# Performance work log

Hardware: AMD Instinct MI355X
Metric: run time of the kernel (lower is better)

Reference implementation:

```python
import jax, jax.numpy as jnp
import numpy as np

N_NODES = 100000
N_EDGES = 1600000
D_FEAT = 48


def setup_inputs() -> dict:
    key = jax.random.key(0)
    k1, k2, k3, k4 = jax.random.split(key, 4)
    rows = jax.random.randint(k1, (N_EDGES,), 0, N_NODES, dtype=jnp.int32)
    cols = jax.random.randint(k2, (N_EDGES,), 0, N_NODES, dtype=jnp.int32)
    vals = jax.random.uniform(k3, (N_EDGES,), dtype=jnp.float32)
    embeds = jax.random.normal(k4, (N_NODES, D_FEAT), dtype=jnp.float32)
    return {"rows": rows, "cols": cols, "vals": vals, "embeds": embeds}


def reference(rows, cols, vals, embeds):
    # out = spmm(adj, embeds): out[r] = sum_{e: rows[e]==r} vals[e] * embeds[cols[e]]
    msgs = vals[:, None] * embeds[cols]  # [E, d] gather + scale
    out = jax.ops.segment_sum(msgs, rows, num_segments=embeds.shape[0])  # [N, d]
    return out
```

## Files before the change

kernel.cpp:

```cpp
#include <hip/hip_runtime.h>
#include <hip/hip_fp16.h>


#define N_NODES 100000
#define N_EDGES 1600000
#define D_FEAT  48

#define RPB 64
#define NBUCKETS ((N_NODES + RPB - 1) / RPB)
#define NWG 256
#define CHUNK ((N_EDGES + NWG - 1) / NWG)
#define MAT (NBUCKETS * NWG)
#define SCAN_CHUNK 2048
#define NB_SCAN ((MAT + SCAN_CHUNK - 1) / SCAN_CHUNK)
#define CONV_N4 ((N_NODES * D_FEAT) / 4)
#define CONV_BLK ((CONV_N4 + 511) / 512)
#define CAP 1536

__global__ __launch_bounds__(512) void count_convert(const int* __restrict__ rows,
                                                     unsigned int* __restrict__ mat,
                                                     const float4* __restrict__ esrc,
                                                     __half2* __restrict__ edst) {
    const int t = threadIdx.x;
    if (blockIdx.x < NWG) {
        __shared__ unsigned int lc[NBUCKETS];
        const int w = blockIdx.x;
        for (int i = t; i < NBUCKETS; i += 512) lc[i] = 0u;
        __syncthreads();
        const int lo = w * CHUNK;
        const int hi = (lo + CHUNK < N_EDGES) ? lo + CHUNK : N_EDGES;
        for (int e = lo + t; e < hi; e += 512)
            atomicAdd(&lc[((unsigned)rows[e]) >> 6], 1u);
        __syncthreads();
        for (int b = t; b < NBUCKETS; b += 512)
            mat[b * NWG + w] = lc[b];
    } else {
        int i = (blockIdx.x - NWG) * 512 + t;
        if (i < CONV_N4) {
            float4 v = esrc[i];
            edst[2 * i]     = __floats2half2_rn(v.x, v.y);
            edst[2 * i + 1] = __floats2half2_rn(v.z, v.w);
        }
    }
}

__global__ __launch_bounds__(256) void scan_phase1(const unsigned int* __restrict__ mat,
                                                   unsigned int* __restrict__ bsum) {
    __shared__ unsigned int s[256];
    const int blk = blockIdx.x, t = threadIdx.x;
    const int base = blk * SCAN_CHUNK + t * 8;
    unsigned int sum = 0;
#pragma unroll
    for (int k = 0; k < 8; ++k) {
        int i = base + k;
        if (i < MAT) sum += mat[i];
    }
    s[t] = sum;
    __syncthreads();
    for (int off = 128; off > 0; off >>= 1) {
        if (t < off) s[t] += s[t + off];
        __syncthreads();
    }
    if (t == 0) bsum[blk] = s[0];
}

__global__ __launch_bounds__(256) void scan_phase3(unsigned int* __restrict__ mat,
                                                   const unsigned int* __restrict__ bsum,
                                                   unsigned int* __restrict__ bstart) {
    __shared__ unsigned int s[256];
    __shared__ unsigned int bpre[256];
    const int blk = blockIdx.x, t = threadIdx.x;
    bpre[t] = (t < NB_SCAN) ? bsum[t] : 0u;
    __syncthreads();
    for (int off = 1; off < 256; off <<= 1) {
        unsigned int u = (t >= off) ? bpre[t - off] : 0u;
        __syncthreads();
        bpre[t] += u;
        __syncthreads();
    }
    const unsigned int blkbase = (blk == 0) ? 0u : bpre[blk - 1];

    const int base = blk * SCAN_CHUNK + t * 8;
    unsigned int c[8];
    unsigned int sum = 0;
#pragma unroll
    for (int k = 0; k < 8; ++k) {
        int i = base + k;
        c[k] = (i < MAT) ? mat[i] : 0u;
        sum += c[k];
    }
    s[t] = sum;
    __syncthreads();
    for (int off = 1; off < 256; off <<= 1) {
        unsigned int u = (t >= off) ? s[t - off] : 0u;
        __syncthreads();
        s[t] += u;
        __syncthreads();
    }
    unsigned int prefix = blkbase + ((t == 0) ? 0u : s[t - 1]);
#pragma unroll
    for (int k = 0; k < 8; ++k) {
        int i = base + k;
        if (i < MAT) {
            mat[i] = prefix;
            if ((i & (NWG - 1)) == 0) bstart[i >> 8] = prefix;
            prefix += c[k];
        }
    }
    if (blk == 0 && t == 0) bstart[NBUCKETS] = N_EDGES;
}

__global__ __launch_bounds__(512) void place_kernel(const int* __restrict__ rows,
                                                    const int* __restrict__ cols,
                                                    const float* __restrict__ vals,
                                                    const unsigned int* __restrict__ mat,
                                                    int2* __restrict__ buf1) {
    __shared__ unsigned int lc[NBUCKETS];
    const int w = blockIdx.x, t = threadIdx.x;
    for (int b = t; b < NBUCKETS; b += 512) lc[b] = mat[b * NWG + w];
    __syncthreads();
    const int lo = w * CHUNK;
    const int hi = (lo + CHUNK < N_EDGES) ? lo + CHUNK : N_EDGES;
    for (int e = lo + t; e < hi; e += 512) {
        unsigned r = (unsigned)rows[e];
        unsigned int pos = atomicAdd(&lc[r >> 6], 1u);
        buf1[pos] = make_int2((int)(((r & 63u) << 17) | (unsigned)cols[e]),
                              __float_as_int(vals[e]));
    }
}

__global__ __launch_bounds__(512) void finalize_spmm(const unsigned int* __restrict__ bstart,
                                                     const int2* __restrict__ buf1,
                                                     const __half2* __restrict__ embeds_h2,
                                                     float* __restrict__ out) {
    __shared__ unsigned int sedge[CAP];
    __shared__ unsigned int rstart[RPB + 1];
    __shared__ unsigned int rc[RPB];
    __shared__ unsigned int sscan[RPB];
    const int b = blockIdx.x, t = threadIdx.x;
    const unsigned int S = bstart[b];
    const unsigned int E = bstart[b + 1];
    const unsigned int cnt = E - S;
    const int g   = t >> 5;
    const int sub = t & 31;
    const bool act = sub < 24;
    const int row0 = b * RPB;

#define PROC(q)                                                       \
    {                                                                 \
        union { __half h; unsigned short u; } hv;                     \
        hv.u = (unsigned short)((q) >> 17);                           \
        float vv = __half2float(hv.h);                                \
        __half2 e2 = embeds_h2[((q) & 0x1FFFFu) * 24 + sub];          \
        ax = fmaf(vv, __low2float(e2), ax);                           \
        ay = fmaf(vv, __high2float(e2), ay);                          \
    }

    if (cnt <= CAP) {
        if (t < RPB) rc[t] = 0u;
        __syncthreads();
        for (unsigned int j = S + t; j < E; j += 512)
            atomicAdd(&rc[(unsigned)buf1[j].x >> 17], 1u);
        __syncthreads();
        if (t < RPB) sscan[t] = rc[t];
        __syncthreads();
        for (int off = 1; off < RPB; off <<= 1) {
            unsigned int u = 0;
            if (t < RPB && t >= off) u = sscan[t - off];
            __syncthreads();
            if (t < RPB && t >= off) sscan[t] += u;
            __syncthreads();
        }
        if (t < RPB) {
            unsigned int pre = (t == 0) ? 0u : sscan[t - 1];
            rstart[t] = pre;
            rc[t] = pre;
        }
        if (t == 0) rstart[RPB] = cnt;
        __syncthreads();
        for (unsigned int j = S + t; j < E; j += 512) {
            int2 cv = buf1[j];
            unsigned int pos = atomicAdd(&rc[(unsigned)cv.x >> 17], 1u);
            union { __half h; unsigned short u; } hv;
            hv.h = __float2half_rn(__int_as_float(cv.y));
            sedge[pos] = ((unsigned int)hv.u << 17) | ((unsigned)cv.x & 0x1FFFFu);
        }
        __syncthreads();

        for (int rr = g * 4; rr < g * 4 + 4; ++rr) {
            int row = row0 + rr;
            if (row >= N_NODES) break;
            unsigned int j = rstart[rr], end = rstart[rr + 1];
            float ax = 0.f, ay = 0.f;
            for (; j + 8 <= end; j += 8) {
                unsigned int q0 = sedge[j + 0];
                unsigned int q1 = sedge[j + 1];
                unsigned int q2 = sedge[j + 2];
                unsigned int q3 = sedge[j + 3];
                unsigned int q4 = sedge[j + 4];
                unsigned int q5 = sedge[j + 5];
                unsigned int q6 = sedge[j + 6];
                unsigned int q7 = sedge[j + 7];
                if (act) {
                    PROC(q0) PROC(q1) PROC(q2) PROC(q3)
                    PROC(q4) PROC(q5) PROC(q6) PROC(q7)
                }
            }
            for (; j < end; ++j) {
                unsigned int q = sedge[j];
                if (act) PROC(q)
            }
            if (act)
                *(float2*)(out + (size_t)row * D_FEAT + sub * 2) = make_float2(ax, ay);
        }
    } else {
        for (int rr = g * 4; rr < g * 4 + 4; ++rr) {
            int row = row0 + rr;
            if (row >= N_NODES) break;
            float ax = 0.f, ay = 0.f;
            for (unsigned int j = S; j < E; ++j) {
                int2 cv = buf1[j];
                if (((unsigned)cv.x >> 17) == (unsigned)rr && act) {
                    union { __half h; unsigned short u; } hv;
                    hv.h = __float2half_rn(__int_as_float(cv.y));
                    unsigned int q = ((unsigned int)hv.u << 17) | ((unsigned)cv.x & 0x1FFFFu);
                    PROC(q)
                }
            }
            if (act)
                *(float2*)(out + (size_t)row * D_FEAT + sub * 2) = make_float2(ax, ay);
        }
    }
#undef PROC
}

__global__ __launch_bounds__(256) void zero_out_kernel(float4* __restrict__ out, int n4) {
    int i = blockIdx.x * 256 + threadIdx.x;
    if (i < n4) out[i] = make_float4(0.f, 0.f, 0.f, 0.f);
}
__global__ __launch_bounds__(256) void spmm_atomic_kernel(const int* __restrict__ rows,
                                                          const int* __restrict__ cols,
                                                          const float* __restrict__ vals,
                                                          const float* __restrict__ embeds,
                                                          float* __restrict__ out) {
    long long tid = (long long)blockIdx.x * 256 + threadIdx.x;
    const long long total = (long long)N_EDGES * 12;
    if (tid >= total) return;
    int e = (int)(tid / 12), q = (int)(tid % 12);
    int r = rows[e], c = cols[e];
    float v = vals[e];
    const float4 emb = *(const float4*)(embeds + (long long)c * D_FEAT + q * 4);
    float* o = out + (long long)r * D_FEAT + q * 4;
    atomicAdd(o + 0, v * emb.x);
    atomicAdd(o + 1, v * emb.y);
    atomicAdd(o + 2, v * emb.z);
    atomicAdd(o + 3, v * emb.w);
}

extern "C" void kernel_launch(void* const* d_in, const int* in_sizes, int n_in,
                              void* d_out, int out_size, void* d_ws, size_t ws_size,
                              hipStream_t stream) {
    const int*   rows   = (const int*)d_in[0];
    const int*   cols   = (const int*)d_in[1];
    const float* vals   = (const float*)d_in[2];
    const float* embeds = (const float*)d_in[3];
    float*       out    = (float*)d_out;

    unsigned int* mat = (unsigned int*)d_ws;
    size_t mat_bytes  = ((size_t)MAT * 4 + 15) & ~(size_t)15;
    unsigned int* bstart = (unsigned int*)((char*)d_ws + mat_bytes);
    size_t bs_bytes   = (((size_t)(NBUCKETS + 1) * 4) + 15) & ~(size_t)15;
    unsigned int* bsum = (unsigned int*)((char*)d_ws + mat_bytes + bs_bytes);
    size_t bsum_bytes = (((size_t)NB_SCAN * 4) + 15) & ~(size_t)15;
    int2* buf1 = (int2*)((char*)d_ws + mat_bytes + bs_bytes + bsum_bytes);
    __half2* embeds_h2 = (__half2*)((char*)buf1 + (size_t)N_EDGES * 8);
    size_t need = mat_bytes + bs_bytes + bsum_bytes +
                  (size_t)N_EDGES * 8 + (size_t)N_NODES * D_FEAT * 2;

    if (ws_size < need) {
        int n4 = out_size / 4;
        zero_out_kernel<<<(n4 + 255) / 256, 256, 0, stream>>>((float4*)out, n4);
        long long total = (long long)N_EDGES * 12;
        spmm_atomic_kernel<<<(int)((total + 255) / 256), 256, 0, stream>>>(rows, cols, vals, embeds, out);
        return;
    }

    count_convert<<<NWG + CONV_BLK, 512, 0, stream>>>(rows, mat,
                                                      (const float4*)embeds, embeds_h2);
    scan_phase1<<<NB_SCAN, 256, 0, stream>>>(mat, bsum);
    scan_phase3<<<NB_SCAN, 256, 0, stream>>>(mat, bsum, bstart);
    place_kernel<<<NWG, 512, 0, stream>>>(rows, cols, vals, mat, buf1);
    finalize_spmm<<<NBUCKETS, 512, 0, stream>>>(bstart, buf1, embeds_h2, out);
}
```

Baseline: 86.97 us.

## Replace global scan and placement passes with per-workgroup local bucket sort

Each of 128 workgroups now builds a histogram of its own edge chunk, scans it locally and scatters its edges into its own slice of the buffer. This removes the two global scan kernels and the separate placement kernel, so the five launches become two. The finalize kernel then collects each bucket's edges from 128 separate runs, one per workgroup, read with four threads per run. In exchange, each bucket's edges are scattered across many small segments, which costs locality and adds offset reads in the finalize stage.

```diff
diff --git a/kernel.cpp b/kernel.cpp
--- a/kernel.cpp
+++ b/kernel.cpp
@@ -8,32 +8,66 @@
 
 #define RPB 64
 #define NBUCKETS ((N_NODES + RPB - 1) / RPB)
-#define NWG 256
-#define CHUNK ((N_EDGES + NWG - 1) / NWG)
-#define MAT (NBUCKETS * NWG)
-#define SCAN_CHUNK 2048
-#define NB_SCAN ((MAT + SCAN_CHUNK - 1) / SCAN_CHUNK)
+#define NWG 128
+#define CHUNK (N_EDGES / NWG)
+#define MROW (NBUCKETS + 1)
 #define CONV_N4 ((N_NODES * D_FEAT) / 4)
 #define CONV_BLK ((CONV_N4 + 511) / 512)
 #define CAP 1536
 
-__global__ __launch_bounds__(512) void count_convert(const int* __restrict__ rows,
+__global__ __launch_bounds__(512) void build_convert(const int* __restrict__ rows,
+                                                     const int* __restrict__ cols,
+                                                     const float* __restrict__ vals,
                                                      unsigned int* __restrict__ mat,
+                                                     int2* __restrict__ buf1,
                                                      const float4* __restrict__ esrc,
                                                      __half2* __restrict__ edst) {
     const int t = threadIdx.x;
     if (blockIdx.x < NWG) {
-        __shared__ unsigned int lc[NBUCKETS];
+        __shared__ unsigned int hist[NBUCKETS];
+        __shared__ unsigned int part[512];
         const int w = blockIdx.x;
-        for (int i = t; i < NBUCKETS; i += 512) lc[i] = 0u;
-        __syncthreads();
-        const int lo = w * CHUNK;
-        const int hi = (lo + CHUNK < N_EDGES) ? lo + CHUNK : N_EDGES;
+        for (int i = t; i < NBUCKETS; i += 512) hist[i] = 0u;
+        __syncthreads();
+        const int lo = w * CHUNK, hi = lo + CHUNK;
         for (int e = lo + t; e < hi; e += 512)
-            atomicAdd(&lc[((unsigned)rows[e]) >> 6], 1u);
-        __syncthreads();
-        for (int b = t; b < NBUCKETS; b += 512)
-            mat[b * NWG + w] = lc[b];
+            atomicAdd(&hist[((unsigned)rows[e]) >> 6], 1u);
+        __syncthreads();
+        unsigned int c[4], sum = 0;
+#pragma unroll
+        for (int k = 0; k < 4; ++k) {
+            int idx = t * 4 + k;
+            c[k] = (idx < NBUCKETS) ? hist[idx] : 0u;
+            sum += c[k];
+        }
+        part[t] = sum;
+        __syncthreads();
+        for (int off = 1; off < 512; off <<= 1) {
+            unsigned int u = (t >= off) ? part[t - off] : 0u;
+            __syncthreads();
+            part[t] += u;
+            __syncthreads();
+        }
+        unsigned int pre = (t == 0) ? 0u : part[t - 1];
+        unsigned int* mrow = mat + (size_t)w * MROW;
+#pragma unroll
+        for (int k = 0; k < 4; ++k) {
+            int idx = t * 4 + k;
+            if (idx < NBUCKETS) {
+                mrow[idx] = pre;
+                hist[idx] = pre;
+                pre += c[k];
+            }
+        }
+        if (t == 0) mrow[NBUCKETS] = CHUNK;
+        __syncthreads();
+        for (int e = lo + t; e < hi; e += 512) {
+            unsigned r = (unsigned)rows[e];
+            unsigned b = r >> 6;
+            unsigned pos = (unsigned)lo + atomicAdd(&hist[b], 1u);
+            buf1[pos] = make_int2((int)(((r & 63u) << 17) | (unsigned)cols[e]),
+                                  __float_as_int(vals[e]));
+        }
     } else {
         int i = (blockIdx.x - NWG) * 512 + t;
         if (i < CONV_N4) {
@@ -44,92 +78,7 @@
     }
 }
 
-__global__ __launch_bounds__(256) void scan_phase1(const unsigned int* __restrict__ mat,
-                                                   unsigned int* __restrict__ bsum) {
-    __shared__ unsigned int s[256];
-    const int blk = blockIdx.x, t = threadIdx.x;
-    const int base = blk * SCAN_CHUNK + t * 8;
-    unsigned int sum = 0;
-#pragma unroll
-    for (int k = 0; k < 8; ++k) {
-        int i = base + k;
-        if (i < MAT) sum += mat[i];
-    }
-    s[t] = sum;
-    __syncthreads();
-    for (int off = 128; off > 0; off >>= 1) {
-        if (t < off) s[t] += s[t + off];
-        __syncthreads();
-    }
-    if (t == 0) bsum[blk] = s[0];
-}
-
-__global__ __launch_bounds__(256) void scan_phase3(unsigned int* __restrict__ mat,
-                                                   const unsigned int* __restrict__ bsum,
-                                                   unsigned int* __restrict__ bstart) {
-    __shared__ unsigned int s[256];
-    __shared__ unsigned int bpre[256];
-    const int blk = blockIdx.x, t = threadIdx.x;
-    bpre[t] = (t < NB_SCAN) ? bsum[t] : 0u;
-    __syncthreads();
-    for (int off = 1; off < 256; off <<= 1) {
-        unsigned int u = (t >= off) ? bpre[t - off] : 0u;
-        __syncthreads();
-        bpre[t] += u;
-        __syncthreads();
-    }
-    const unsigned int blkbase = (blk == 0) ? 0u : bpre[blk - 1];
-
-    const int base = blk * SCAN_CHUNK + t * 8;
-    unsigned int c[8];
-    unsigned int sum = 0;
-#pragma unroll
-    for (int k = 0; k < 8; ++k) {
-        int i = base + k;
-        c[k] = (i < MAT) ? mat[i] : 0u;
-        sum += c[k];
-    }
-    s[t] = sum;
-    __syncthreads();
-    for (int off = 1; off < 256; off <<= 1) {
-        unsigned int u = (t >= off) ? s[t - off] : 0u;
-        __syncthreads();
-        s[t] += u;
-        __syncthreads();
-    }
-    unsigned int prefix = blkbase + ((t == 0) ? 0u : s[t - 1]);
-#pragma unroll
-    for (int k = 0; k < 8; ++k) {
-        int i = base + k;
-        if (i < MAT) {
-            mat[i] = prefix;
-            if ((i & (NWG - 1)) == 0) bstart[i >> 8] = prefix;
-            prefix += c[k];
-        }
-    }
-    if (blk == 0 && t == 0) bstart[NBUCKETS] = N_EDGES;
-}
-
-__global__ __launch_bounds__(512) void place_kernel(const int* __restrict__ rows,
-                                                    const int* __restrict__ cols,
-                                                    const float* __restrict__ vals,
-                                                    const unsigned int* __restrict__ mat,
-                                                    int2* __restrict__ buf1) {
-    __shared__ unsigned int lc[NBUCKETS];
-    const int w = blockIdx.x, t = threadIdx.x;
-    for (int b = t; b < NBUCKETS; b += 512) lc[b] = mat[b * NWG + w];
-    __syncthreads();
-    const int lo = w * CHUNK;
-    const int hi = (lo + CHUNK < N_EDGES) ? lo + CHUNK : N_EDGES;
-    for (int e = lo + t; e < hi; e += 512) {
-        unsigned r = (unsigned)rows[e];
-        unsigned int pos = atomicAdd(&lc[r >> 6], 1u);
-        buf1[pos] = make_int2((int)(((r & 63u) << 17) | (unsigned)cols[e]),
-                              __float_as_int(vals[e]));
-    }
-}
-
-__global__ __launch_bounds__(512) void finalize_spmm(const unsigned int* __restrict__ bstart,
+__global__ __launch_bounds__(512) void finalize_spmm(const unsigned int* __restrict__ mat,
                                                      const int2* __restrict__ buf1,
                                                      const __half2* __restrict__ embeds_h2,
                                                      float* __restrict__ out) {
@@ -138,9 +87,12 @@
     __shared__ unsigned int rc[RPB];
     __shared__ unsigned int sscan[RPB];
     const int b = blockIdx.x, t = threadIdx.x;
-    const unsigned int S = bstart[b];
-    const unsigned int E = bstart[b + 1];
-    const unsigned int cnt = E - S;
+    const int run  = t >> 2;
+    const int sub4 = t & 3;
+    const unsigned int* mr = mat + (size_t)run * MROW + b;
+    const unsigned int s  = mr[0];
+    const unsigned int e2 = mr[1];
+    const unsigned int base = (unsigned)run * CHUNK;
     const int g   = t >> 5;
     const int sub = t & 31;
     const bool act = sub < 24;
@@ -151,35 +103,37 @@
         union { __half h; unsigned short u; } hv;                     \
         hv.u = (unsigned short)((q) >> 17);                           \
         float vv = __half2float(hv.h);                                \
-        __half2 e2 = embeds_h2[((q) & 0x1FFFFu) * 24 + sub];          \
-        ax = fmaf(vv, __low2float(e2), ax);                           \
-        ay = fmaf(vv, __high2float(e2), ay);                          \
-    }
+        __half2 e2v = embeds_h2[((q) & 0x1FFFFu) * 24 + sub];         \
+        ax = fmaf(vv, __low2float(e2v), ax);                          \
+        ay = fmaf(vv, __high2float(e2v), ay);                         \
+    }
+
+    if (t < RPB) rc[t] = 0u;
+    __syncthreads();
+    for (unsigned int k = s + sub4; k < e2; k += 4)
+        atomicAdd(&rc[(unsigned)buf1[base + k].x >> 17], 1u);
+    __syncthreads();
+    if (t < RPB) sscan[t] = rc[t];
+    __syncthreads();
+    for (int off = 1; off < RPB; off <<= 1) {
+        unsigned int u = 0;
+        if (t < RPB && t >= off) u = sscan[t - off];
+        __syncthreads();
+        if (t < RPB && t >= off) sscan[t] += u;
+        __syncthreads();
+    }
+    if (t < RPB) {
+        unsigned int pre = (t == 0) ? 0u : sscan[t - 1];
+        rstart[t] = pre;
+        rc[t] = pre;
+    }
+    if (t == 0) rstart[RPB] = sscan[RPB - 1];
+    __syncthreads();
+    const unsigned int cnt = rstart[RPB];
 
     if (cnt <= CAP) {
-        if (t < RPB) rc[t] = 0u;
-        __syncthreads();
-        for (unsigned int j = S + t; j < E; j += 512)
-            atomicAdd(&rc[(unsigned)buf1[j].x >> 17], 1u);
-        __syncthreads();
-        if (t < RPB) sscan[t] = rc[t];
-        __syncthreads();
-        for (int off = 1; off < RPB; off <<= 1) {
-            unsigned int u = 0;
-            if (t < RPB && t >= off) u = sscan[t - off];
-            __syncthreads();
-            if (t < RPB && t >= off) sscan[t] += u;
-            __syncthreads();
-        }
-        if (t < RPB) {
-            unsigned int pre = (t == 0) ? 0u : sscan[t - 1];
-            rstart[t] = pre;
-            rc[t] = pre;
-        }
-        if (t == 0) rstart[RPB] = cnt;
-        __syncthreads();
-        for (unsigned int j = S + t; j < E; j += 512) {
-            int2 cv = buf1[j];
+        for (unsigned int k = s + sub4; k < e2; k += 4) {
+            int2 cv = buf1[base + k];
             unsigned int pos = atomicAdd(&rc[(unsigned)cv.x >> 17], 1u);
             union { __half h; unsigned short u; } hv;
             hv.h = __float2half_rn(__int_as_float(cv.y));
@@ -218,13 +172,17 @@
             int row = row0 + rr;
             if (row >= N_NODES) break;
             float ax = 0.f, ay = 0.f;
-            for (unsigned int j = S; j < E; ++j) {
-                int2 cv = buf1[j];
-                if (((unsigned)cv.x >> 17) == (unsigned)rr && act) {
-                    union { __half h; unsigned short u; } hv;
-                    hv.h = __float2half_rn(__int_as_float(cv.y));
-                    unsigned int q = ((unsigned int)hv.u << 17) | ((unsigned)cv.x & 0x1FFFFu);
-                    PROC(q)
+            for (int i = 0; i < NWG; ++i) {
+                const unsigned int* mri = mat + (size_t)i * MROW + b;
+                unsigned int si = mri[0], ei = mri[1];
+                for (unsigned int k = si; k < ei; ++k) {
+                    int2 cv = buf1[(unsigned)i * CHUNK + k];
+                    if (((unsigned)cv.x >> 17) == (unsigned)rr && act) {
+                        union { __half h; unsigned short u; } hv;
+                        hv.h = __float2half_rn(__int_as_float(cv.y));
+                        unsigned int q = ((unsigned int)hv.u << 17) | ((unsigned)cv.x & 0x1FFFFu);
+                        PROC(q)
+                    }
                 }
             }
             if (act)
@@ -267,15 +225,10 @@
     float*       out    = (float*)d_out;
 
     unsigned int* mat = (unsigned int*)d_ws;
-    size_t mat_bytes  = ((size_t)MAT * 4 + 15) & ~(size_t)15;
-    unsigned int* bstart = (unsigned int*)((char*)d_ws + mat_bytes);
-    size_t bs_bytes   = (((size_t)(NBUCKETS + 1) * 4) + 15) & ~(size_t)15;
-    unsigned int* bsum = (unsigned int*)((char*)d_ws + mat_bytes + bs_bytes);
-    size_t bsum_bytes = (((size_t)NB_SCAN * 4) + 15) & ~(size_t)15;
-    int2* buf1 = (int2*)((char*)d_ws + mat_bytes + bs_bytes + bsum_bytes);
+    size_t mat_bytes  = ((size_t)NWG * MROW * 4 + 15) & ~(size_t)15;
+    int2* buf1 = (int2*)((char*)d_ws + mat_bytes);
     __half2* embeds_h2 = (__half2*)((char*)buf1 + (size_t)N_EDGES * 8);
-    size_t need = mat_bytes + bs_bytes + bsum_bytes +
-                  (size_t)N_EDGES * 8 + (size_t)N_NODES * D_FEAT * 2;
+    size_t need = mat_bytes + (size_t)N_EDGES * 8 + (size_t)N_NODES * D_FEAT * 2;
 
     if (ws_size < need) {
         int n4 = out_size / 4;
@@ -285,10 +238,7 @@
         return;
     }
 
-    count_convert<<<NWG + CONV_BLK, 512, 0, stream>>>(rows, mat,
+    build_convert<<<NWG + CONV_BLK, 512, 0, stream>>>(rows, cols, vals, mat, buf1,
                                                       (const float4*)embeds, embeds_h2);
-    scan_phase1<<<NB_SCAN, 256, 0, stream>>>(mat, bsum);
-    scan_phase3<<<NB_SCAN, 256, 0, stream>>>(mat, bsum, bstart);
-    place_kernel<<<NWG, 512, 0, stream>>>(rows, cols, vals, mat, buf1);
-    finalize_spmm<<<NBUCKETS, 512, 0, stream>>>(bstart, buf1, embeds_h2, out);
-}
+    finalize_spmm<<<NBUCKETS, 512, 0, stream>>>(mat, buf1, embeds_h2, out);
+}
```

Result: faster. 83.02 us (-4.5%).
